# Kernel tuning notes

Measured on AMD Instinct MI355X. Metric: run time of the kernel, lower is better.

## Reference

```python
import jax, jax.numpy as jnp
import numpy as np

M_DIM = 32          # vec_dim m
L1 = L2 = L3 = L4 = 3
L_TOT = L1 * L2 * L3 * L4   # 81
R = 2               # rank1..rank4 window size
B_SZ = 4
D_SZ = 16           # D1 = D2 = D3 = D4


def _make_bbasis():
    # Bbasis[idx, i] = prod_k cos(2*pi*(j_k+1)/(i+2)), idx = flattened (j1,j2,j3,j4)
    i = jnp.arange(M_DIM, dtype=jnp.float32)
    def c(Lk):
        j = jnp.arange(Lk, dtype=jnp.float32)
        return jnp.cos(2.0 * jnp.pi * (j[:, None] + 1.0) / (i[None, :] + 2.0))  # [Lk, m]
    c1, c2, c3, c4 = c(L1), c(L2), c(L3), c(L4)
    Bb = (c1[:, None, None, None, :] * c2[None, :, None, None, :]
          * c3[None, None, :, None, :] * c4[None, None, None, :, :])
    return Bb.reshape(L_TOT, M_DIM)


def _window_basis_idx(n1, n2, n3, n4):
    # linear mode, drop: window top-left coords are 0..n_k-1 with step 1
    j1 = jnp.arange(n1) % L1
    j2 = jnp.arange(n2) % L2
    j3 = jnp.arange(n3) % L3
    j4 = jnp.arange(n4) % L4
    idx = (((j1[:, None, None, None] * L2 + j2[None, :, None, None]) * L3
            + j3[None, None, :, None]) * L4 + j4[None, None, None, :])
    return idx.reshape(-1)  # [n_windows]


def setup_inputs() -> dict:
    key = jax.random.key(0)
    k1, k2, k3 = jax.random.split(key, 3)
    arr_batch = jax.random.normal(k1, (B_SZ, D_SZ, D_SZ, D_SZ, D_SZ, M_DIM), dtype=jnp.float32)
    # M initialized near identity (nn.init.eye_ + perturbation so grads are non-trivial)
    M = jnp.eye(M_DIM, dtype=jnp.float32) + 0.01 * jax.random.normal(k2, (M_DIM, M_DIM), dtype=jnp.float32)
    # Acoeff ~ U(-0.1, 0.1) as in reset_parameters
    Acoeff = jax.random.uniform(k3, (M_DIM, L_TOT), dtype=jnp.float32, minval=-0.1, maxval=0.1)
    Bbasis = _make_bbasis()  # fixed buffer, computed deterministically
    return {"arr_batch": arr_batch, "M": M, "Acoeff": Acoeff, "Bbasis": Bbasis}


def reference(arr_batch, M, Acoeff, Bbasis):
    Bsz, D1, D2, D3, D4, m = arr_batch.shape
    # map every vector through M (x @ M.T); avg-pooling commutes with the linear map,
    # matching `mapped = windows @ M.T` then mean over the window
    mapped = jnp.einsum('bpqrsm,nm->bpqrsn', arr_batch, M)
    # 4D sliding window (rank=2 per dim, stride 1, 'drop' -> VALID), rank_op='avg'
    win = (1, R, R, R, R, 1)
    agg = jax.lax.reduce_window(mapped, 0.0, jax.lax.add, win, (1,) * 6, 'VALID') / float(R ** 4)
    n1, n2, n3, n4 = agg.shape[1:5]
    n_win = n1 * n2 * n3 * n4
    agg = agg.reshape(Bsz, n_win, m)            # [B, W, m]
    idx = _window_basis_idx(n1, n2, n3, n4)     # [W]
    phi = Bbasis[idx]                           # [W, m]
    # t_k = Acoeff[:, j_k] * (Bbasis[j_k, :] . agg_k); representation = mean_k t_k
    s = jnp.einsum('bwm,wm->bw', agg, phi)      # [B, W]
    t = s[:, :, None] * Acoeff.T[idx][None]     # [B, W, m]
    return t.mean(axis=1)                       # [B, m]
```

## Files before the change

kernel.cpp:

```cpp
#include <hip/hip_runtime.h>


static __device__ __forceinline__ void add4(float4& a, const float4& b) {
    a.x += b.x; a.y += b.y; a.z += b.z; a.w += b.w;
}
static __device__ __forceinline__ void fma4(float4& a, float w, const float4& b) {
    a.x = fmaf(w, b.x, a.x); a.y = fmaf(w, b.y, a.y);
    a.z = fmaf(w, b.z, a.z); a.w = fmaf(w, b.w, a.w);
}

__global__ __launch_bounds__(128) void sdd4_stage1(
    const float* __restrict__ arr,
    const float* __restrict__ Mmat,
    const float* __restrict__ Bbasis,
    float* __restrict__ S)
{
    __shared__ float4 U_lds[400];
    __shared__ float  V_lds[9 * 33];
    __shared__ float  Y_lds[9 * 33];
    __shared__ float  M_lds[32 * 33];
    __shared__ float  B_lds[81 * 33];

    const int t  = threadIdx.x;
    const int bx = blockIdx.x;
    const int b  = bx >> 8;
    const int p  = (bx >> 4) & 15;
    const int q  = bx & 15;

    const float4* M4 = reinterpret_cast<const float4*>(Mmat);
    for (int i = t; i < 256; i += 128) {
        float4 v = M4[i];
        float* dst = &M_lds[(i >> 3) * 33 + (i & 7) * 4];
        dst[0] = v.x; dst[1] = v.y; dst[2] = v.z; dst[3] = v.w;
    }
    const float4* B4 = reinterpret_cast<const float4*>(Bbasis);
    for (int i = t; i < 648; i += 128) {
        float4 v = B4[i];
        float* dst = &B_lds[(i >> 3) * 33 + (i & 7) * 4];
        dst[0] = v.x; dst[1] = v.y; dst[2] = v.z; dst[3] = v.w;
    }

    const int r  = t >> 3;
    const int mv = t & 7;
    const float4* A4 = reinterpret_cast<const float4*>(arr);
    const size_t tile = (size_t)((b * 16 + p) * 16 + q) * 2048;

    float4 u0 = make_float4(0.f, 0.f, 0.f, 0.f), u1 = u0, u2 = u0;
    #pragma unroll
    for (int s = 0; s < 16; ++s) {
        float4 x = A4[tile + (size_t)(r * 16 + s) * 8 + mv];
        if ((0x36DBu >> s) & 1) add4(u0, x);
        if ((0x6DB6u >> s) & 1) add4(u1, x);
        if ((0xDB6Cu >> s) & 1) add4(u2, x);
    }
    U_lds[r * 25 +      mv] = u0;
    U_lds[r * 25 +  8 + mv] = u1;
    U_lds[r * 25 + 16 + mv] = u2;
    __syncthreads();

    if (t < 72) {
        const int j3  = t / 24;
        const int rem = t % 24;
        const int j4  = rem >> 3;
        const int mv2 = rem & 7;
        const unsigned msk = (j3 == 0) ? 0x36DBu : (j3 == 1 ? 0x6DB6u : 0xDB6Cu);
        float4 acc = make_float4(0.f, 0.f, 0.f, 0.f);
        #pragma unroll
        for (int rr = 0; rr < 16; ++rr) {
            float w = (float)((msk >> rr) & 1u);
            fma4(acc, w, U_lds[rr * 25 + j4 * 8 + mv2]);
        }
        const int jj = j3 * 3 + j4;
        float* dv = &V_lds[jj * 33 + mv2 * 4];
        dv[0] = acc.x; dv[1] = acc.y; dv[2] = acc.z; dv[3] = acc.w;
    }
    __syncthreads();

    for (int o = t; o < 288; o += 128) {
        const int jj = o >> 5;
        const int n  = o & 31;
        float acc = 0.f;
        #pragma unroll
        for (int m = 0; m < 32; ++m)
            acc = fmaf(M_lds[n * 33 + m], V_lds[jj * 33 + m], acc);
        Y_lds[jj * 33 + n] = acc;
    }
    __syncthreads();

    int l1_0, l1_1 = 0, n1;
    if      (p == 0)  { l1_0 = 0; n1 = 1; }
    else if (p == 15) { l1_0 = 2; n1 = 1; }
    else              { l1_0 = (p - 1) % 3; l1_1 = p % 3; n1 = 2; }
    int l2_0, l2_1 = 0, n2;
    if      (q == 0)  { l2_0 = 0; n2 = 1; }
    else if (q == 15) { l2_0 = 2; n2 = 1; }
    else              { l2_0 = (q - 1) % 3; l2_1 = q % 3; n2 = 2; }

    const int ncomb = n1 * n2 * 9;
    if (t < ncomb) {
        const int jj  = t % 9;
        const int c12 = t / 9;
        const int i1idx = (n2 == 2) ? (c12 >> 1) : c12;
        const int i2idx = (n2 == 2) ? (c12 & 1)  : 0;
        const int i1 = i1idx ? l1_1 : l1_0;
        const int i2 = i2idx ? l2_1 : l2_0;
        const int jf = (i1 * 3 + i2) * 9 + jj;
        float acc = 0.f;
        #pragma unroll
        for (int n = 0; n < 32; ++n)
            acc = fmaf(Y_lds[jj * 33 + n], B_lds[jf * 33 + n], acc);
        atomicAdd(&S[b * 81 + jf], acc);
    }
}

__global__ __launch_bounds__(128) void sdd4_stage2(
    const float* __restrict__ S,
    const float* __restrict__ Acoeff,
    float* __restrict__ out)
{
    const int t = threadIdx.x;
    const int b = t >> 5;
    const int n = t & 31;
    float acc = 0.f;
    #pragma unroll
    for (int j = 0; j < 81; ++j)
        acc = fmaf(Acoeff[n * 81 + j], S[b * 81 + j], acc);
    out[b * 32 + n] = acc * (1.0f / 810000.0f);
}

extern "C" void kernel_launch(void* const* d_in, const int* in_sizes, int n_in,
                              void* d_out, int out_size, void* d_ws, size_t ws_size,
                              hipStream_t stream) {
    const float* arr    = (const float*)d_in[0];
    const float* Mmat   = (const float*)d_in[1];
    const float* Acoeff = (const float*)d_in[2];
    const float* Bbasis = (const float*)d_in[3];
    float* S = (float*)d_ws;

    hipMemsetAsync(d_ws, 0, 4 * 81 * sizeof(float), stream);
    sdd4_stage1<<<dim3(1024), dim3(128), 0, stream>>>(arr, Mmat, Bbasis, S);
    sdd4_stage2<<<dim3(1), dim3(128), 0, stream>>>(S, Acoeff, (float*)d_out);
}
```

Baseline: 87.16 us.

## Precompute Bbasis·M once, replace atomics with per-block partials and reduction

Adds a one-block stage that forms Bbasis·M once, so each stage-1 block loads this product and skips the per-block M mapping stage and one barrier. Stage 1 now writes an 81-entry partial per block, with zeros for unused entries, instead of doing atomicAdds into a memset workspace, which also removes the memset call. Stage 2 reduces the partials per batch across 4 blocks. In exchange there is an extra kernel launch, a serial dependency on the tiny precompute kernel, and extra global traffic for the partials.

Measured after the change: 94.04 us. +7.9%, slower.

```diff
diff --git a/kernel.cpp b/kernel.cpp
--- a/kernel.cpp
+++ b/kernel.cpp
@@ -9,17 +9,39 @@
     a.z = fmaf(w, b.z, a.z); a.w = fmaf(w, b.w, a.w);
 }
 
+__global__ __launch_bounds__(256) void sdd4_stage0(
+    const float* __restrict__ Mmat,
+    const float* __restrict__ Bbasis,
+    float* __restrict__ BM)
+{
+    __shared__ float M_lds[32 * 33];
+    const int t = threadIdx.x;
+    {
+        const float4* M4 = reinterpret_cast<const float4*>(Mmat);
+        float4 v = M4[t];
+        float* dst = &M_lds[(t >> 3) * 33 + (t & 7) * 4];
+        dst[0] = v.x; dst[1] = v.y; dst[2] = v.z; dst[3] = v.w;
+    }
+    __syncthreads();
+    for (int o = t; o < 2592; o += 256) {
+        const int j = o >> 5;
+        const int m = o & 31;
+        float acc = 0.f;
+        #pragma unroll
+        for (int n = 0; n < 32; ++n)
+            acc = fmaf(Bbasis[j * 32 + n], M_lds[n * 33 + m], acc);
+        BM[o] = acc;
+    }
+}
+
 __global__ __launch_bounds__(128) void sdd4_stage1(
     const float* __restrict__ arr,
-    const float* __restrict__ Mmat,
-    const float* __restrict__ Bbasis,
-    float* __restrict__ S)
+    const float* __restrict__ BM,
+    float* __restrict__ P)
 {
     __shared__ float4 U_lds[400];
     __shared__ float  V_lds[9 * 33];
-    __shared__ float  Y_lds[9 * 33];
-    __shared__ float  M_lds[32 * 33];
-    __shared__ float  B_lds[81 * 33];
+    __shared__ float  BM_lds[81 * 33];
 
     const int t  = threadIdx.x;
     const int bx = blockIdx.x;
@@ -27,16 +49,10 @@
     const int p  = (bx >> 4) & 15;
     const int q  = bx & 15;
 
-    const float4* M4 = reinterpret_cast<const float4*>(Mmat);
-    for (int i = t; i < 256; i += 128) {
-        float4 v = M4[i];
-        float* dst = &M_lds[(i >> 3) * 33 + (i & 7) * 4];
-        dst[0] = v.x; dst[1] = v.y; dst[2] = v.z; dst[3] = v.w;
-    }
-    const float4* B4 = reinterpret_cast<const float4*>(Bbasis);
+    const float4* BM4 = reinterpret_cast<const float4*>(BM);
     for (int i = t; i < 648; i += 128) {
-        float4 v = B4[i];
-        float* dst = &B_lds[(i >> 3) * 33 + (i & 7) * 4];
+        float4 v = BM4[i];
+        float* dst = &BM_lds[(i >> 3) * 33 + (i & 7) * 4];
         dst[0] = v.x; dst[1] = v.y; dst[2] = v.z; dst[3] = v.w;
     }
 
@@ -76,56 +92,56 @@
     }
     __syncthreads();
 
-    for (int o = t; o < 288; o += 128) {
-        const int jj = o >> 5;
-        const int n  = o & 31;
+    if (t < 81) {
+        const int i1 = t / 27;
+        const int i2 = (t / 9) % 3;
+        const int jj = t % 9;
+        const bool ok1 = (p == 0)  ? (i1 == 0)
+                       : (p == 15) ? (i1 == 2)
+                       : (i1 == (p - 1) % 3 || i1 == p % 3);
+        const bool ok2 = (q == 0)  ? (i2 == 0)
+                       : (q == 15) ? (i2 == 2)
+                       : (i2 == (q - 1) % 3 || i2 == q % 3);
         float acc = 0.f;
-        #pragma unroll
-        for (int m = 0; m < 32; ++m)
-            acc = fmaf(M_lds[n * 33 + m], V_lds[jj * 33 + m], acc);
-        Y_lds[jj * 33 + n] = acc;
-    }
-    __syncthreads();
-
-    int l1_0, l1_1 = 0, n1;
-    if      (p == 0)  { l1_0 = 0; n1 = 1; }
-    else if (p == 15) { l1_0 = 2; n1 = 1; }
-    else              { l1_0 = (p - 1) % 3; l1_1 = p % 3; n1 = 2; }
-    int l2_0, l2_1 = 0, n2;
-    if      (q == 0)  { l2_0 = 0; n2 = 1; }
-    else if (q == 15) { l2_0 = 2; n2 = 1; }
-    else              { l2_0 = (q - 1) % 3; l2_1 = q % 3; n2 = 2; }
-
-    const int ncomb = n1 * n2 * 9;
-    if (t < ncomb) {
-        const int jj  = t % 9;
-        const int c12 = t / 9;
-        const int i1idx = (n2 == 2) ? (c12 >> 1) : c12;
-        const int i2idx = (n2 == 2) ? (c12 & 1)  : 0;
-        const int i1 = i1idx ? l1_1 : l1_0;
-        const int i2 = i2idx ? l2_1 : l2_0;
-        const int jf = (i1 * 3 + i2) * 9 + jj;
-        float acc = 0.f;
-        #pragma unroll
-        for (int n = 0; n < 32; ++n)
-            acc = fmaf(Y_lds[jj * 33 + n], B_lds[jf * 33 + n], acc);
-        atomicAdd(&S[b * 81 + jf], acc);
+        if (ok1 && ok2) {
+            #pragma unroll
+            for (int m = 0; m < 32; ++m)
+                acc = fmaf(BM_lds[t * 33 + m], V_lds[jj * 33 + m], acc);
+        }
+        P[bx * 81 + t] = acc;
     }
 }
 
-__global__ __launch_bounds__(128) void sdd4_stage2(
-    const float* __restrict__ S,
+__global__ __launch_bounds__(256) void sdd4_stage2(
+    const float* __restrict__ P,
     const float* __restrict__ Acoeff,
     float* __restrict__ out)
 {
+    __shared__ float Sp[3 * 81];
+    __shared__ float Sf[81];
     const int t = threadIdx.x;
-    const int b = t >> 5;
-    const int n = t & 31;
-    float acc = 0.f;
-    #pragma unroll
-    for (int j = 0; j < 81; ++j)
-        acc = fmaf(Acoeff[n * 81 + j], S[b * 81 + j], acc);
-    out[b * 32 + n] = acc * (1.0f / 810000.0f);
+    const int b = blockIdx.x;
+
+    if (t < 243) {
+        const int g  = t / 81;
+        const int jf = t - g * 81;
+        const float* base = P + (size_t)(b * 256) * 81 + jf;
+        float acc = 0.f;
+        #pragma unroll 4
+        for (int r = g; r < 256; r += 3)
+            acc += base[(size_t)r * 81];
+        Sp[g * 81 + jf] = acc;
+    }
+    __syncthreads();
+    if (t < 81) Sf[t] = Sp[t] + Sp[81 + t] + Sp[162 + t];
+    __syncthreads();
+    if (t < 32) {
+        float acc = 0.f;
+        #pragma unroll
+        for (int j = 0; j < 81; ++j)
+            acc = fmaf(Acoeff[t * 81 + j], Sf[j], acc);
+        out[b * 32 + t] = acc * (1.0f / 810000.0f);
+    }
 }
 
 extern "C" void kernel_launch(void* const* d_in, const int* in_sizes, int n_in,
@@ -135,9 +151,11 @@
     const float* Mmat   = (const float*)d_in[1];
     const float* Acoeff = (const float*)d_in[2];
     const float* Bbasis = (const float*)d_in[3];
-    float* S = (float*)d_ws;
 
-    hipMemsetAsync(d_ws, 0, 4 * 81 * sizeof(float), stream);
-    sdd4_stage1<<<dim3(1024), dim3(128), 0, stream>>>(arr, Mmat, Bbasis, S);
-    sdd4_stage2<<<dim3(1), dim3(128), 0, stream>>>(S, Acoeff, (float*)d_out);
+    float* BM = (float*)d_ws;
+    float* P  = (float*)d_ws + 4096;
+
+    sdd4_stage0<<<dim3(1),    dim3(256), 0, stream>>>(Mmat, Bbasis, BM);
+    sdd4_stage1<<<dim3(1024), dim3(128), 0, stream>>>(arr, BM, P);
+    sdd4_stage2<<<dim3(4),    dim3(256), 0, stream>>>(P, Acoeff, (float*)d_out);
 }
```
